# Kernel tuning notes

Measured on AMD Instinct MI355X. Metric: run time of the kernel, lower is better.

## Reference

```python
import jax, jax.numpy as jnp
import numpy as np

Q_MAX = 127.0  # 2^(8-1) - 1 for 8-bit activations


def _ste_round(x):
    # forward: round(x); backward: identity
    return x + jax.lax.stop_gradient(jnp.round(x) - x)


def setup_inputs() -> dict:
    key = jax.random.key(0)
    k1, k2 = jax.random.split(key)
    B, S, D_IN, D_OUT = 4, 4096, 2048, 2048
    x = jax.random.normal(k1, (B, S, D_IN), dtype=jnp.float32)
    # muP-style init: std = 1/sqrt(fan_in)
    weight = jax.random.normal(k2, (D_OUT, D_IN), dtype=jnp.float32) / np.sqrt(D_IN)
    return {"x": x, "weight": weight}


def reference(x, weight):
    # --- ternary weight quantization (AbsMean) ---
    w_scale = jnp.maximum(jnp.mean(jnp.abs(weight)), 1e-6)        # scalar
    w_norm = weight / w_scale
    w_quant = jnp.clip(_ste_round(w_norm), -1.0, 1.0)             # [O, I], values in {-1,0,1}

    # --- per-token absmax activation quantization (8-bit) ---
    a_scale = jnp.clip(jnp.max(jnp.abs(x), axis=-1, keepdims=True), 1e-8, None)  # [B,S,1]
    x_quant = jnp.clip(_ste_round(x * (Q_MAX / a_scale)), -Q_MAX, Q_MAX)         # [B,S,I]

    # --- scaled matmul: y = (x_q @ w_q^T) * w_scale * (a_scale / Q_MAX) ---
    y = jnp.einsum('bsi,oi->bso', x_quant, w_quant)
    y = y * (w_scale * (a_scale / Q_MAX))
    return y
```

## Files before the change

### kernel.cpp

```cpp
#include <hip/hip_runtime.h>
#include <hip/hip_bf16.h>

typedef int int4v __attribute__((ext_vector_type(4)));

#define K_DIM 2048
#define N_DIM 2048
#define M_DIM 16384
#define NW 4194304
#define BKB 128
#define NKT (K_DIM / BKB)

__global__ void k_wsum(const float4* __restrict__ w4, double* __restrict__ red) {
  const int n4 = NW / 4;
  double s = 0.0;
  for (int i = blockIdx.x * blockDim.x + threadIdx.x; i < n4; i += gridDim.x * blockDim.x) {
    float4 v = w4[i];
    s += (double)fabsf(v.x) + (double)fabsf(v.y) + (double)fabsf(v.z) + (double)fabsf(v.w);
  }
  for (int o = 32; o; o >>= 1) s += __shfl_xor(s, o);
  __shared__ double sd[4];
  if ((threadIdx.x & 63) == 0) sd[threadIdx.x >> 6] = s;
  __syncthreads();
  if (threadIdx.x == 0) red[blockIdx.x] = (sd[0] + sd[1]) + (sd[2] + sd[3]);
}

__global__ void k_wscale(const double* __restrict__ red, double* __restrict__ wsd) {
  double s = 0.0;
  for (int i = 0; i < 256; ++i) s += red[i];
  double m = s / (double)NW;
  *wsd = (m > 1e-6) ? m : 1e-6;
}

__device__ __forceinline__ char wq1(float v, double ws) {
  double r = rint((double)v / ws);
  r = fmin(fmax(r, -1.0), 1.0);
  return (char)(int)r;
}

__global__ void k_wquant(const float4* __restrict__ w4, const double* __restrict__ wsd,
                         char4* __restrict__ wq4) {
  int i = blockIdx.x * blockDim.x + threadIdx.x;
  if (i >= NW / 4) return;
  double ws = *wsd;
  float4 v = w4[i];
  char4 q;
  q.x = wq1(v.x, ws);
  q.y = wq1(v.y, ws);
  q.z = wq1(v.z, ws);
  q.w = wq1(v.w, ws);
  wq4[i] = q;
}

__device__ __forceinline__ char qi8(float v, double rr) {
  double q = rint((double)v * rr);
  q = fmin(fmax(q, -127.0), 127.0);
  return (char)(int)q;
}

__global__ void k_xquant(const float* __restrict__ x, float* __restrict__ ascale,
                         char* __restrict__ xq) {
  const int row = blockIdx.x;
  const int t = threadIdx.x;
  const float4* xr = (const float4*)(x + (size_t)row * K_DIM);
  float4 v0 = xr[t];
  float4 v1 = xr[t + 256];
  float m = fmaxf(fmaxf(fmaxf(fabsf(v0.x), fabsf(v0.y)), fmaxf(fabsf(v0.z), fabsf(v0.w))),
                  fmaxf(fmaxf(fabsf(v1.x), fabsf(v1.y)), fmaxf(fabsf(v1.z), fabsf(v1.w))));
  for (int o = 32; o; o >>= 1) m = fmaxf(m, __shfl_xor(m, o));
  __shared__ float sm[4];
  if ((t & 63) == 0) sm[t >> 6] = m;
  __syncthreads();
  float a = fmaxf(fmaxf(sm[0], sm[1]), fmaxf(sm[2], sm[3]));
  a = fmaxf(a, 1e-8f);
  if (t == 0) ascale[row] = a;
  double rr = 127.0 / (double)a;
  char4* qr4 = (char4*)(xq + (size_t)row * K_DIM);
  char4 a4, b4;
  a4.x = qi8(v0.x, rr); a4.y = qi8(v0.y, rr); a4.z = qi8(v0.z, rr); a4.w = qi8(v0.w, rr);
  b4.x = qi8(v1.x, rr); b4.y = qi8(v1.y, rr); b4.z = qi8(v1.z, rr); b4.w = qi8(v1.w, rr);
  qr4[t] = a4;
  qr4[t + 256] = b4;
}

__device__ __forceinline__ void gload16(const void* g, void* l) {
  __builtin_amdgcn_global_load_lds(
      (const __attribute__((address_space(1))) void*)g,
      (__attribute__((address_space(3))) void*)l, 16, 0, 0);
}

#define STAGE2(SRC, DST, C0, C1)              \
  gload16((SRC) + soff[C0], (DST) + loff[C0]); \
  gload16((SRC) + soff[C1], (DST) + loff[C1]);

#define READ_A(MH, CO)                                        \
  _Pragma("unroll") for (int mf = 0; mf < 4; ++mf) {          \
    int row = rA + (MH)*64 + mf * 16;                         \
    af[mf] = *(const int4v*)(cA + row * 128 + (CO));          \
  }

#define READ_B(CO)                                            \
  _Pragma("unroll") for (int nf = 0; nf < 4; ++nf) {          \
    int row = rB + nf * 16;                                   \
    bfr[nf] = *(const int4v*)(cB + row * 128 + (CO));         \
  }

#define MFMA16(MH)                                                             \
  __builtin_amdgcn_s_setprio(1);                                               \
  _Pragma("unroll") for (int mf = 0; mf < 4; ++mf)                             \
  _Pragma("unroll") for (int nf = 0; nf < 4; ++nf)                             \
    acc[(MH)*4 + mf][nf] = __builtin_amdgcn_mfma_i32_16x16x64_i8(              \
        af[mf], bfr[nf], acc[(MH)*4 + mf][nf], 0, 0, 0);                       \
  __builtin_amdgcn_s_setprio(0);

#define FENCE_LGKM0                                          \
  asm volatile("s_waitcnt lgkmcnt(0)" ::: "memory");         \
  __builtin_amdgcn_sched_barrier(0);

__global__ __launch_bounds__(512, 2) void k_gemm(
    const char* __restrict__ xq, const char* __restrict__ wq,
    const float* __restrict__ ascale, const double* __restrict__ wsd,
    float* __restrict__ out) {
  __shared__ __align__(16) char lds[131072];
  char* lA0 = lds;
  char* lB0 = lds + 32768;
  char* lA1 = lds + 65536;
  char* lB1 = lds + 98304;

  const int tid = threadIdx.x;
  const int l = tid & 63;
  const int wv = tid >> 6;
  const int wm = wv >> 2;
  const int wn = wv & 3;
  const int g = l >> 4, r16 = l & 15;

  const int bid = blockIdx.x;
  const int logical = (bid & 7) * 64 + (bid >> 3);
  const int br = logical >> 3;
  const int bc = logical & 7;

  const char* Ab = xq + (size_t)br * 256 * K_DIM;
  const char* Bb = wq + (size_t)bc * 256 * K_DIM;

  int soff[4], loff[4];
#pragma unroll
  for (int c = 0; c < 4; ++c) {
    int lb = c * 8192 + tid * 16;
    loff[c] = lb;
    int row = lb >> 7;
    int cb = lb & 127;
    soff[c] = row * K_DIM + (cb ^ ((row & 7) << 4));
  }

  const int sw = (r16 & 7) << 4;
  const int co0 = (g * 16) ^ sw;
  const int co1 = (64 + g * 16) ^ sw;
  const int rA = wm * 128 + r16;
  const int rB = wn * 64 + r16;

  int4v acc[8][4];
#pragma unroll
  for (int mf = 0; mf < 8; ++mf)
#pragma unroll
    for (int nf = 0; nf < 4; ++nf) acc[mf][nf] = (int4v){0, 0, 0, 0};

#pragma unroll
  for (int c = 0; c < 4; ++c) gload16(Ab + soff[c], lA0 + loff[c]);
#pragma unroll
  for (int c = 0; c < 4; ++c) gload16(Bb + soff[c], lB0 + loff[c]);

  char* cA = lA0; char* cB = lB0;
  char* nA = lA1; char* nB = lB1;

  for (int kt = 0; kt < NKT; ++kt) {
    const int kn = ((kt + 1) & (NKT - 1)) * BKB;
    const char* An = Ab + kn;
    const char* Bn = Bb + kn;
    int4v af[4], bfr[4];

    STAGE2(An, nA, 0, 1);
    asm volatile("s_waitcnt vmcnt(2)" ::: "memory");
    __builtin_amdgcn_s_barrier();
    asm volatile("" ::: "memory");
    READ_A(0, co0);
    READ_B(co0);
    FENCE_LGKM0;
    MFMA16(0);

    STAGE2(An, nA, 2, 3);
    READ_A(1, co0);
    FENCE_LGKM0;
    MFMA16(1);

    STAGE2(Bn, nB, 0, 1);
    READ_A(0, co1);
    READ_B(co1);
    FENCE_LGKM0;
    MFMA16(0);

    STAGE2(Bn, nB, 2, 3);
    READ_A(1, co1);
    FENCE_LGKM0;
    MFMA16(1);

    asm volatile("" ::: "memory");
    __builtin_amdgcn_s_barrier();
    asm volatile("" ::: "memory");

    char* t;
    t = cA; cA = nA; nA = t;
    t = cB; cB = nB; nB = t;
  }

  float wsf = (float)(*wsd);
  size_t trow0 = (size_t)br * 256 + wm * 128;
  int oc0 = bc * 256 + wn * 64;
#pragma unroll
  for (int mf = 0; mf < 8; ++mf) {
#pragma unroll
    for (int j = 0; j < 4; ++j) {
      size_t t = trow0 + mf * 16 + g * 4 + j;
      float s = wsf * (ascale[t] / 127.0f);
      float* yr = out + t * (size_t)N_DIM + oc0;
#pragma unroll
      for (int nf = 0; nf < 4; ++nf) yr[nf * 16 + r16] = (float)acc[mf][nf][j] * s;
    }
  }
}

extern "C" void kernel_launch(void* const* d_in, const int* in_sizes, int n_in,
                              void* d_out, int out_size, void* d_ws, size_t ws_size,
                              hipStream_t stream) {
  const float* x = (const float*)d_in[0];
  const float* w = (const float*)d_in[1];
  float* out = (float*)d_out;

  char* ws = (char*)d_ws;
  double* red = (double*)ws;
  double* wsd = (double*)(ws + 2048);
  float* ascale = (float*)(ws + 4096);
  char* xq = (char*)(ws + 4096 + 65536);
  char* wq = xq + (size_t)M_DIM * K_DIM;

  k_wsum<<<256, 256, 0, stream>>>((const float4*)w, red);
  k_wscale<<<1, 1, 0, stream>>>(red, wsd);
  k_wquant<<<NW / 4 / 256, 256, 0, stream>>>((const float4*)w, wsd, (char4*)wq);
  k_xquant<<<M_DIM, 256, 0, stream>>>(x, ascale, xq);
  k_gemm<<<dim3(N_DIM / 256 * M_DIM / 256), 512, 0, stream>>>(xq, wq, ascale, wsd, out);
}
```

Before: 131.2 us.

## Restructure GEMM k-loop with register double-buffered fragments and one-barrier prefetch

The GEMM main loop is unrolled by two with fixed LDS buffers. Each k-tile now issues the whole next-tile prefetch up front after a single vmcnt(0) wait and barrier, and the final redundant prefetch is skipped. Register fragments are double-buffered (afA/afB, bfA/bfB) so LDS reads overlap the MFMA groups without explicit lgkmcnt(0) fences. It also parallelizes the scalar weight-scale reduction from one thread to 256. The trade-offs are a full vmcnt(0) wait before each tile, and higher register pressure from the extra fragment buffers at 2 blocks per CU.

```diff
diff --git a/kernel.cpp b/kernel.cpp
--- a/kernel.cpp
+++ b/kernel.cpp
@@ -25,10 +25,15 @@
 }
 
 __global__ void k_wscale(const double* __restrict__ red, double* __restrict__ wsd) {
-  double s = 0.0;
-  for (int i = 0; i < 256; ++i) s += red[i];
-  double m = s / (double)NW;
-  *wsd = (m > 1e-6) ? m : 1e-6;
+  double s = red[threadIdx.x];
+  for (int o = 32; o; o >>= 1) s += __shfl_xor(s, o);
+  __shared__ double sd[4];
+  if ((threadIdx.x & 63) == 0) sd[threadIdx.x >> 6] = s;
+  __syncthreads();
+  if (threadIdx.x == 0) {
+    double m = ((sd[0] + sd[1]) + (sd[2] + sd[3])) / (double)NW;
+    *wsd = (m > 1e-6) ? m : 1e-6;
+  }
 }
 
 __device__ __forceinline__ char wq1(float v, double ws) {
@@ -88,33 +93,46 @@
       (__attribute__((address_space(3))) void*)l, 16, 0, 0);
 }
 
-#define STAGE2(SRC, DST, C0, C1)              \
-  gload16((SRC) + soff[C0], (DST) + loff[C0]); \
-  gload16((SRC) + soff[C1], (DST) + loff[C1]);
-
-#define READ_A(MH, CO)                                        \
-  _Pragma("unroll") for (int mf = 0; mf < 4; ++mf) {          \
-    int row = rA + (MH)*64 + mf * 16;                         \
-    af[mf] = *(const int4v*)(cA + row * 128 + (CO));          \
-  }
-
-#define READ_B(CO)                                            \
-  _Pragma("unroll") for (int nf = 0; nf < 4; ++nf) {          \
-    int row = rB + nf * 16;                                   \
-    bfr[nf] = *(const int4v*)(cB + row * 128 + (CO));         \
-  }
-
-#define MFMA16(MH)                                                             \
-  __builtin_amdgcn_s_setprio(1);                                               \
-  _Pragma("unroll") for (int mf = 0; mf < 4; ++mf)                             \
-  _Pragma("unroll") for (int nf = 0; nf < 4; ++nf)                             \
-    acc[(MH)*4 + mf][nf] = __builtin_amdgcn_mfma_i32_16x16x64_i8(              \
-        af[mf], bfr[nf], acc[(MH)*4 + mf][nf], 0, 0, 0);                       \
+#define RD_A(DST, CA, MH, CO)                                               \
+  _Pragma("unroll") for (int mf = 0; mf < 4; ++mf)                          \
+    DST[mf] = *(const int4v*)((CA) + (rA + (MH)*64 + mf * 16) * 128 + (CO));
+
+#define RD_B(DST, CB, CO)                                                   \
+  _Pragma("unroll") for (int nf = 0; nf < 4; ++nf)                          \
+    DST[nf] = *(const int4v*)((CB) + (rB + nf * 16) * 128 + (CO));
+
+#define MM(MH, AF, BF)                                                      \
+  __builtin_amdgcn_s_setprio(1);                                            \
+  _Pragma("unroll") for (int mf = 0; mf < 4; ++mf)                          \
+  _Pragma("unroll") for (int nf = 0; nf < 4; ++nf)                          \
+    acc[(MH)*4 + mf][nf] = __builtin_amdgcn_mfma_i32_16x16x64_i8(           \
+        AF[mf], BF[nf], acc[(MH)*4 + mf][nf], 0, 0, 0);                     \
   __builtin_amdgcn_s_setprio(0);
 
-#define FENCE_LGKM0                                          \
-  asm volatile("s_waitcnt lgkmcnt(0)" ::: "memory");         \
-  __builtin_amdgcn_sched_barrier(0);
+#define KTILE(KT, CA, CB, NA, NB, DOSTAGE)                                  \
+  {                                                                         \
+    asm volatile("s_waitcnt vmcnt(0)" ::: "memory");                        \
+    __builtin_amdgcn_s_barrier();                                           \
+    asm volatile("" ::: "memory");                                          \
+    if (DOSTAGE) {                                                          \
+      const char* An = Ab + ((KT) + 1) * BKB;                               \
+      const char* Bn = Bb + ((KT) + 1) * BKB;                               \
+      _Pragma("unroll") for (int c = 0; c < 4; ++c)                         \
+        gload16(An + soff[c], (NA) + loff[c]);                              \
+      _Pragma("unroll") for (int c = 0; c < 4; ++c)                         \
+        gload16(Bn + soff[c], (NB) + loff[c]);                              \
+    }                                                                       \
+    RD_A(afA, CA, 0, co0);                                                  \
+    RD_B(bfA, CB, co0);                                                     \
+    RD_A(afB, CA, 1, co0);         \
+    MM(0, afA, bfA);                                                        \
+    RD_A(afA, CA, 0, co1);                                   \
+    RD_B(bfB, CB, co1);                                                     \
+    MM(1, afB, bfA);                                                        \
+    RD_A(afB, CA, 1, co1);                                   \
+    MM(0, afA, bfB);                                                        \
+    MM(1, afB, bfB);                                                        \
+  }
 
 __global__ __launch_bounds__(512, 2) void k_gemm(
     const char* __restrict__ xq, const char* __restrict__ wq,
@@ -168,47 +186,11 @@
 #pragma unroll
   for (int c = 0; c < 4; ++c) gload16(Bb + soff[c], lB0 + loff[c]);
 
-  char* cA = lA0; char* cB = lB0;
-  char* nA = lA1; char* nB = lB1;
-
-  for (int kt = 0; kt < NKT; ++kt) {
-    const int kn = ((kt + 1) & (NKT - 1)) * BKB;
-    const char* An = Ab + kn;
-    const char* Bn = Bb + kn;
-    int4v af[4], bfr[4];
-
-    STAGE2(An, nA, 0, 1);
-    asm volatile("s_waitcnt vmcnt(2)" ::: "memory");
-    __builtin_amdgcn_s_barrier();
-    asm volatile("" ::: "memory");
-    READ_A(0, co0);
-    READ_B(co0);
-    FENCE_LGKM0;
-    MFMA16(0);
-
-    STAGE2(An, nA, 2, 3);
-    READ_A(1, co0);
-    FENCE_LGKM0;
-    MFMA16(1);
-
-    STAGE2(Bn, nB, 0, 1);
-    READ_A(0, co1);
-    READ_B(co1);
-    FENCE_LGKM0;
-    MFMA16(0);
-
-    STAGE2(Bn, nB, 2, 3);
-    READ_A(1, co1);
-    FENCE_LGKM0;
-    MFMA16(1);
-
-    asm volatile("" ::: "memory");
-    __builtin_amdgcn_s_barrier();
-    asm volatile("" ::: "memory");
-
-    char* t;
-    t = cA; cA = nA; nA = t;
-    t = cB; cB = nB; nB = t;
+  int4v afA[4], afB[4], bfA[4], bfB[4];
+
+  for (int kt = 0; kt < NKT; kt += 2) {
+    KTILE(kt,     lA0, lB0, lA1, lB1, true);
+    KTILE(kt + 1, lA1, lB1, lA0, lB0, (kt + 2 < NKT));
   }
 
   float wsf = (float)(*wsd);
@@ -242,7 +224,7 @@
   char* wq = xq + (size_t)M_DIM * K_DIM;
 
   k_wsum<<<256, 256, 0, stream>>>((const float4*)w, red);
-  k_wscale<<<1, 1, 0, stream>>>(red, wsd);
+  k_wscale<<<1, 256, 0, stream>>>(red, wsd);
   k_wquant<<<NW / 4 / 256, 256, 0, stream>>>((const float4*)w, wsd, (char4*)wq);
   k_xquant<<<M_DIM, 256, 0, stream>>>(x, ascale, xq);
   k_gemm<<<dim3(N_DIM / 256 * M_DIM / 256), 512, 0, stream>>>(xq, wq, ascale, wsd, out);
```

New measurement: 150.6 us. +14.7%, slower.
